# Optimization experiments

Hardware: AMD Instinct MI355X
Metric: run time of the kernel (lower is better)

The kernel has to match this reference:

```python
import jax, jax.numpy as jnp
import numpy as np

B, T, D_IN, H, D_ENC, P, D_ATT = 64, 20, 512, 512, 2048, 196, 512


def setup_inputs() -> dict:
    key = jax.random.key(0)
    ks = jax.random.split(key, 12)
    s = 0.05  # weight scale to keep gates out of saturation
    return {
        "x": jax.random.normal(ks[0], (B, T, D_IN), jnp.float32),
        "cnn_features": jax.random.normal(ks[1], (B, P, D_ENC), jnp.float32),
        "Wi": jax.random.normal(ks[2], (D_IN + H + D_ENC, H), jnp.float32) * s,
        "bi": jnp.zeros((H,), jnp.float32),
        "Wf": jax.random.normal(ks[3], (D_IN + H + D_ENC, H), jnp.float32) * s,
        "bf": jnp.zeros((H,), jnp.float32),
        "Wc": jax.random.normal(ks[4], (D_IN + H + D_ENC, H), jnp.float32) * s,
        "bc": jnp.zeros((H,), jnp.float32),
        "Wo": jax.random.normal(ks[5], (D_IN + H + D_ENC, H), jnp.float32) * s,
        "bo": jnp.zeros((H,), jnp.float32),
        "Wa_feat": jax.random.normal(ks[6], (D_ENC, D_ATT), jnp.float32) * s,
        "Wa_h": jax.random.normal(ks[7], (H, D_ATT), jnp.float32) * s,
        "ba": jnp.zeros((D_ATT,), jnp.float32),
        "v": jax.random.normal(ks[8], (D_ATT,), jnp.float32) * s,
    }


def reference(x, cnn_features, Wi, bi, Wf, bf, Wc, bc, Wo, bo, Wa_feat, Wa_h, ba, v):
    batch, seq_len, _ = x.shape
    hid = Wi.shape[1]
    # feature projection is h-independent: hoist out of the time loop
    feat_proj = jnp.einsum('bpe,ea->bpa', cnn_features, Wa_feat) + ba  # [B,P,A]

    def step(carry, x_t):
        h, c = carry
        # additive (Bahdanau) attention over pixels
        e = jnp.einsum('bpa,a->bp', jnp.tanh(feat_proj + (h @ Wa_h)[:, None, :]), v)
        alpha = jax.nn.softmax(e, axis=-1)                      # [B,P]
        ctx = jnp.einsum('bp,bpe->be', alpha, cnn_features)     # [B,E]
        comb = jnp.concatenate([x_t, h, ctx], axis=1)           # [B,D_IN+H+E]
        i_t = jax.nn.sigmoid(comb @ Wi + bi)
        f_t = jax.nn.sigmoid(comb @ Wf + bf)
        o_t = jax.nn.sigmoid(comb @ Wo + bo)
        c_tilde = jnp.tanh(comb @ Wc + bc)
        c_new = f_t * c + i_t * c_tilde
        h_new = o_t * jnp.tanh(c_new)
        return (h_new, c_new), h_new

    h0 = jnp.zeros((batch, hid), x.dtype)
    c0 = jnp.zeros((batch, hid), x.dtype)
    (h_T, c_T), ys = jax.lax.scan(step, (h0, c0), jnp.swapaxes(x, 0, 1))
    outputs = jnp.swapaxes(ys, 0, 1)  # [B,T,H]
    return outputs, h_T, c_T
```

## Files before the change

kernel.cpp:

```cpp
#include <hip/hip_runtime.h>

typedef unsigned short u16;
typedef unsigned int u32;
typedef __attribute__((ext_vector_type(8))) short bf16x8;
typedef __attribute__((ext_vector_type(4))) float f32x4;

#define NB 64
#define NT 20
#define NH 512
#define NP 196
#define NE 2048
#define NA 512

__device__ __forceinline__ u16 f2bf(float f) {
  u32 b = __float_as_uint(f);
  return (u16)((b + 0x7FFFu + ((b >> 16) & 1u)) >> 16);
}
__device__ __forceinline__ float bf2f(u16 u) { return __uint_as_float(((u32)u) << 16); }
__device__ __forceinline__ float tanh_fast(float x) {
  float xc = fminf(fmaxf(x, -15.f), 15.f);
  float e2 = __builtin_amdgcn_exp2f(xc * 2.885390082f);
  return (e2 - 1.f) * __builtin_amdgcn_rcpf(e2 + 1.f);
}
__device__ __forceinline__ float sigmoid_fast(float x) {
  return __builtin_amdgcn_rcpf(1.f + __builtin_amdgcn_exp2f(x * -1.44269504f));
}

__global__ __launch_bounds__(256) void conv_bf16(const float4* __restrict__ src,
                                                 u16* __restrict__ dst, int n4) {
  int i = blockIdx.x * 256 + threadIdx.x;
  int stride = gridDim.x * 256;
  for (; i < n4; i += stride) {
    float4 v = src[i];
    u32 lo = (u32)f2bf(v.x) | ((u32)f2bf(v.y) << 16);
    u32 hi = (u32)f2bf(v.z) | ((u32)f2bf(v.w) << 16);
    *(uint2*)(dst + (size_t)i * 4) = make_uint2(lo, hi);
  }
}

__global__ __launch_bounds__(128) void conv_x(const float* __restrict__ x,
                                              u16* __restrict__ xbT) {
  int b = blockIdx.x, t = blockIdx.y, tid = threadIdx.x;
  float4 v = *(const float4*)(x + ((size_t)b * NT + t) * 512 + tid * 4);
  u32 lo = (u32)f2bf(v.x) | ((u32)f2bf(v.y) << 16);
  u32 hi = (u32)f2bf(v.z) | ((u32)f2bf(v.w) << 16);
  *(uint2*)(xbT + ((size_t)t * NB + b) * 512 + tid * 4) = make_uint2(lo, hi);
}

__global__ __launch_bounds__(256) void transpose_w(const float* __restrict__ W0,
                                                   const float* __restrict__ W1,
                                                   const float* __restrict__ W2,
                                                   const float* __restrict__ W3,
                                                   u16* __restrict__ dst, int row_off, int K) {
  const float* src = blockIdx.z == 0 ? W0 : blockIdx.z == 1 ? W1 : blockIdx.z == 2 ? W2 : W3;
  __shared__ float tile[32][33];
  int k0 = blockIdx.x * 32, n0 = blockIdx.y * 32;
  int tx = threadIdx.x & 31, ty = threadIdx.x >> 5;
#pragma unroll
  for (int i = 0; i < 4; ++i)
    tile[ty + i * 8][tx] = src[(size_t)(row_off + k0 + ty + i * 8) * 512 + n0 + tx];
  __syncthreads();
#pragma unroll
  for (int i = 0; i < 4; ++i) {
    int n = n0 + ty + i * 8, k = k0 + tx;
    dst[((size_t)blockIdx.z * 512 + n) * K + k] = f2bf(tile[tx][ty + i * 8]);
  }
}

template <bool OUT_BF16, bool BIAS, bool REMAP>
__global__ __launch_bounds__(256) void gemm_bf16(const u16* __restrict__ A,
                                                 const u16* __restrict__ BT,
                                                 const float* __restrict__ bias,
                                                 void* __restrict__ Cout, int M, int N, int K) {
  __shared__ u16 lA[128 * 64];
  __shared__ u16 lB[128 * 64];
  const int tid = threadIdx.x;
  const int lane = tid & 63;
  const int wid = tid >> 6;
  const int m0 = blockIdx.x * 128, n0 = blockIdx.y * 128;
  const int wm = (wid >> 1) * 64, wn = (wid & 1) * 64;
  f32x4 acc[4][4] = {};

  for (int k0 = 0; k0 < K; k0 += 64) {
    __syncthreads();
#pragma unroll
    for (int it = 0; it < 4; ++it) {
      int c = tid + it * 256;
      int r = c >> 3, c7 = c & 7;
      uint4 va = *(const uint4*)(A + (size_t)(m0 + r) * K + k0 + c7 * 8);
      uint4 vb = *(const uint4*)(BT + (size_t)(n0 + r) * K + k0 + c7 * 8);
      int ldsoff = r * 64 + ((c7 ^ (r & 7)) * 8);
      *(uint4*)(lA + ldsoff) = va;
      *(uint4*)(lB + ldsoff) = vb;
    }
    __syncthreads();
#pragma unroll
    for (int kk = 0; kk < 2; ++kk) {
      int kchunk = kk * 4 + (lane >> 4);
      bf16x8 af[4], bg[4];
#pragma unroll
      for (int i = 0; i < 4; ++i) {
        int row = wm + i * 16 + (lane & 15);
        af[i] = *(const bf16x8*)(lA + row * 64 + ((kchunk ^ (row & 7)) * 8));
        int rowb = wn + i * 16 + (lane & 15);
        bg[i] = *(const bf16x8*)(lB + rowb * 64 + ((kchunk ^ (rowb & 7)) * 8));
      }
#pragma unroll
      for (int i = 0; i < 4; ++i)
#pragma unroll
        for (int j = 0; j < 4; ++j)
          acc[i][j] = __builtin_amdgcn_mfma_f32_16x16x32_bf16(af[i], bg[j], acc[i][j], 0, 0, 0);
    }
  }
#pragma unroll
  for (int i = 0; i < 4; ++i) {
    int m = m0 + wm + i * 16 + ((lane >> 4) * 4);
#pragma unroll
    for (int j = 0; j < 4; ++j) {
      int n = n0 + wn + j * 16 + (lane & 15);
      float bv = BIAS ? bias[n] : 0.f;
#pragma unroll
      for (int r = 0; r < 4; ++r) {
        float val = acc[i][j][r] + bv;
        if (REMAP) {
          u32 me = (u32)(m + r);
          u32 bdx = me / 196u;
          u32 p = me - bdx * 196u;
          u32 g = (u32)n >> 9;
          u32 n9 = (u32)n & 511u;
          ((u16*)Cout)[(((size_t)bdx * 4 + g) * 196 + p) * 512 + n9] = f2bf(val);
        } else if (OUT_BF16) {
          ((u16*)Cout)[(size_t)(m + r) * N + n] = f2bf(val);
        } else {
          ((float*)Cout)[(size_t)(m + r) * N + n] = val;
        }
      }
    }
  }
}

__global__ __launch_bounds__(256) void hproj(const u16* __restrict__ hprev,
                                             const u16* __restrict__ wcT,
                                             float* __restrict__ hp) {
  const int ntile = blockIdx.x;
  const int tid = threadIdx.x, lane = tid & 63, kh = tid >> 6;
  const int l15 = lane & 15;
  const u16* Bp = wcT + (size_t)(ntile * 16 + l15) * 512 + kh * 128 + ((lane >> 4) * 8);
  const u16* Ap = hprev + (size_t)l15 * 512 + kh * 128 + ((lane >> 4) * 8);
  f32x4 acc[4] = {};
#pragma unroll
  for (int ks = 0; ks < 4; ++ks) {
    bf16x8 bb = *(const bf16x8*)(Bp + ks * 32);
#pragma unroll
    for (int mf = 0; mf < 4; ++mf) {
      bf16x8 a = *(const bf16x8*)(Ap + (size_t)mf * 16 * 512 + ks * 32);
      acc[mf] = __builtin_amdgcn_mfma_f32_16x16x32_bf16(a, bb, acc[mf], 0, 0, 0);
    }
  }
  __shared__ float pre[4][64][16];
  const int rrow = (lane >> 4) * 4;
#pragma unroll
  for (int mf = 0; mf < 4; ++mf)
#pragma unroll
    for (int r = 0; r < 4; ++r) pre[kh][mf * 16 + rrow + r][l15] = acc[mf][r];
  __syncthreads();
  const int m = tid >> 2, n = (tid & 3) * 4;
  float4 s;
  float* sp = (float*)&s;
#pragma unroll
  for (int j = 0; j < 4; ++j)
    sp[j] = pre[0][m][n + j] + pre[1][m][n + j] + pre[2][m][n + j] + pre[3][m][n + j];
  *(float4*)(hp + (size_t)m * 2560 + ntile * 16 + n) = s;
}

__global__ __launch_bounds__(1024) void attn_gates(
    const u16* __restrict__ fpb, const float* __restrict__ hp, const float* __restrict__ v,
    const u16* __restrict__ cw, const float* __restrict__ xw, const float* __restrict__ bi,
    const float* __restrict__ bfg, const float* __restrict__ bc, const float* __restrict__ bo,
    float* __restrict__ cbuf, float* __restrict__ out, u16* __restrict__ hnext, int t) {
  const int b = blockIdx.x & 63;
  const int half = blockIdx.x >> 6;
  const int tid = threadIdx.x;
  const int lane = tid & 63, wid = tid >> 6;
  __shared__ float smem_a[1024];
  __shared__ float sm[256];
  __shared__ float alp[200];
  __shared__ float red[8192];

  float* hwa = smem_a;
  float* vv = smem_a + 512;
  if (tid < 512) {
    hwa[tid] = (t > 0) ? hp[(size_t)b * 2560 + 2048 + tid] : 0.f;
    vv[tid] = v[tid];
  }
  if (tid >= 196 && tid < 256) red[tid] = -3e38f;
  __syncthreads();

  float hw[8], vr[8];
#pragma unroll
  for (int j = 0; j < 8; ++j) {
    hw[j] = hwa[lane * 8 + j];
    vr[j] = vv[lane * 8 + j];
  }
  for (int p = wid; p < NP; p += 16) {
    const u16* fp = fpb + ((size_t)b * NP + p) * 512 + lane * 8;
    uint4 raw = *(const uint4*)fp;
    u32 w[4] = {raw.x, raw.y, raw.z, raw.w};
    float part = 0.f;
#pragma unroll
    for (int j = 0; j < 8; ++j) {
      u16 u = (u16)(w[j >> 1] >> ((j & 1) * 16));
      part += tanh_fast(bf2f(u) + hw[j]) * vr[j];
    }
#pragma unroll
    for (int off = 32; off > 0; off >>= 1) part += __shfl_xor(part, off);
    if (lane == 0) red[p] = part;
  }
  __syncthreads();

  float ev = (tid < 256) ? red[tid] : -3e38f;
  if (tid < 256) sm[tid] = ev;
  __syncthreads();
  for (int s = 128; s > 0; s >>= 1) {
    if (tid < s) sm[tid] = fmaxf(sm[tid], sm[tid + s]);
    __syncthreads();
  }
  float mx = sm[0];
  __syncthreads();
  float w = (tid < NP) ? __builtin_amdgcn_exp2f((ev - mx) * 1.44269504f) : 0.f;
  if (tid < 256) sm[tid] = w;
  __syncthreads();
  for (int s = 128; s > 0; s >>= 1) {
    if (tid < s) sm[tid] += sm[tid + s];
    __syncthreads();
  }
  float inv = __builtin_amdgcn_rcpf(sm[0]);
  if (tid < NP) alp[tid] = w * inv;
  __syncthreads();

  {
    const int g = tid >> 8, pg = (tid >> 5) & 7, colc = tid & 31;
    const u16* base = cw + ((size_t)(b * 4 + g) * 196) * 512 + half * 256 + colc * 8;
    float acc[8] = {};
    for (int i = 0; i < 25; ++i) {
      int p = pg + i * 8;
      if (p < NP) {
        float al = alp[p];
        uint4 raw = *(const uint4*)(base + (size_t)p * 512);
        u32 wds[4] = {raw.x, raw.y, raw.z, raw.w};
#pragma unroll
        for (int j = 0; j < 8; ++j) acc[j] += al * bf2f((u16)(wds[j >> 1] >> ((j & 1) * 16)));
      }
    }
#pragma unroll
    for (int j = 0; j < 8; ++j) red[((g * 8 + pg) * 32 + colc) * 8 + j] = acc[j];
  }
  __syncthreads();

  float* pre4 = smem_a;
  {
    const int g = tid >> 8, nn = tid & 255;
    float s = 0.f;
#pragma unroll
    for (int pg = 0; pg < 8; ++pg) s += red[((g * 8 + pg) * 32 + (nn >> 3)) * 8 + (nn & 7)];
    pre4[g * 256 + nn] = s;
  }
  __syncthreads();

  if (tid < 256) {
    const int ng = half * 256 + tid;
    const size_t xwo = ((size_t)t * NB + b) * 2048;
    const size_t hpb = (size_t)b * 2560;
    float hwh0 = 0.f, hwh1 = 0.f, hwh2 = 0.f, hwh3 = 0.f;
    if (t > 0) {
      hwh0 = hp[hpb + ng];
      hwh1 = hp[hpb + 512 + ng];
      hwh2 = hp[hpb + 1024 + ng];
      hwh3 = hp[hpb + 1536 + ng];
    }
    float ip = pre4[0 * 256 + tid] + xw[xwo + ng] + hwh0 + bi[ng];
    float fp = pre4[1 * 256 + tid] + xw[xwo + 512 + ng] + hwh1 + bfg[ng];
    float cp = pre4[2 * 256 + tid] + xw[xwo + 1024 + ng] + hwh2 + bc[ng];
    float op = pre4[3 * 256 + tid] + xw[xwo + 1536 + ng] + hwh3 + bo[ng];
    float it = sigmoid_fast(ip), ft = sigmoid_fast(fp), ot = sigmoid_fast(op);
    float ctl = tanh_fast(cp);
    float cold = (t > 0) ? cbuf[(size_t)b * 512 + ng] : 0.f;
    float cn = ft * cold + it * ctl;
    float hn = ot * tanh_fast(cn);
    cbuf[(size_t)b * 512 + ng] = cn;
    hnext[(size_t)b * 512 + ng] = f2bf(hn);
    out[((size_t)b * NT + t) * 512 + ng] = hn;
    if (t == NT - 1) {
      out[(size_t)NB * NT * 512 + (size_t)b * 512 + ng] = hn;
      out[(size_t)NB * NT * 512 + (size_t)NB * 512 + (size_t)b * 512 + ng] = cn;
    }
  }
}

extern "C" void kernel_launch(void* const* d_in, const int* in_sizes, int n_in, void* d_out,
                              int out_size, void* d_ws, size_t ws_size, hipStream_t stream) {
  const float* x = (const float*)d_in[0];
  const float* cnn = (const float*)d_in[1];
  const float* Wi = (const float*)d_in[2];
  const float* bi = (const float*)d_in[3];
  const float* Wf = (const float*)d_in[4];
  const float* bfv = (const float*)d_in[5];
  const float* Wc = (const float*)d_in[6];
  const float* bc = (const float*)d_in[7];
  const float* Wo = (const float*)d_in[8];
  const float* bo = (const float*)d_in[9];
  const float* Waf = (const float*)d_in[10];
  const float* Wah = (const float*)d_in[11];
  const float* ba = (const float*)d_in[12];
  const float* v = (const float*)d_in[13];
  float* out = (float*)d_out;

  char* base = (char*)d_ws;
  size_t off = 0;
  auto alloc = [&](size_t bytes) {
    char* r = base + off;
    off += (bytes + 255) & ~(size_t)255;
    return r;
  };
  u16* cnnb = (u16*)alloc((size_t)NB * NP * NE * 2);
  u16* fpb = (u16*)alloc((size_t)NB * NP * NA * 2);
  u16* cnW = (u16*)alloc((size_t)NB * 4 * NP * 512 * 2);
  u16* wctxT = (u16*)alloc((size_t)4 * 512 * 2048 * 2);
  u16* wcombT = (u16*)alloc((size_t)2560 * 512 * 2);
  u16* wxt = (u16*)alloc((size_t)4 * 512 * 512 * 2);
  u16* waft = (u16*)alloc((size_t)512 * 2048 * 2);
  u16* xbT = (u16*)alloc((size_t)NT * NB * 512 * 2);
  float* xw = (float*)alloc((size_t)NT * NB * 2048 * 4);
  u16* hbuf = (u16*)alloc((size_t)2 * NB * 512 * 2);
  float* cbuf = (float*)alloc((size_t)NB * 512 * 4);
  float* hp = (float*)alloc((size_t)NB * 2560 * 4);

  (void)ws_size;
  (void)in_sizes;
  (void)n_in;
  (void)out_size;

  conv_bf16<<<2048, 256, 0, stream>>>((const float4*)cnn, cnnb, (NB * NP * NE) / 4);
  conv_x<<<dim3(NB, NT), 128, 0, stream>>>(x, xbT);
  {
    dim3 g1(512 / 32, 16, 4);
    transpose_w<<<g1, 256, 0, stream>>>(Wi, Wf, Wc, Wo, wxt, 0, 512);
    dim3 g2(2048 / 32, 16, 1);
    transpose_w<<<g2, 256, 0, stream>>>(Waf, Waf, Waf, Waf, waft, 0, 2048);
    dim3 g3(2048 / 32, 16, 4);
    transpose_w<<<g3, 256, 0, stream>>>(Wi, Wf, Wc, Wo, wctxT, 1024, 2048);
    dim3 g4(512 / 32, 16, 4);
    transpose_w<<<g4, 256, 0, stream>>>(Wi, Wf, Wc, Wo, wcombT, 512, 512);
    dim3 g5(512 / 32, 16, 1);
    transpose_w<<<g5, 256, 0, stream>>>(Wah, Wah, Wah, Wah, wcombT + (size_t)2048 * 512, 0, 512);
  }

  {
    dim3 g(12544 / 128, 512 / 128);
    gemm_bf16<true, true, false><<<g, 256, 0, stream>>>(cnnb, waft, ba, fpb, 12544, 512, 2048);
  }
  {
    dim3 g(1280 / 128, 2048 / 128);
    gemm_bf16<false, false, false><<<g, 256, 0, stream>>>(xbT, wxt, nullptr, xw, 1280, 2048, 512);
  }
  {
    dim3 g(12544 / 128, 2048 / 128);
    gemm_bf16<true, false, true><<<g, 256, 0, stream>>>(cnnb, wctxT, nullptr, cnW, 12544, 2048,
                                                        2048);
  }

  for (int t = 0; t < NT; ++t) {
    const u16* hprev = hbuf + (size_t)(t & 1) * NB * 512;
    u16* hnext = hbuf + (size_t)((t + 1) & 1) * NB * 512;
    if (t > 0) hproj<<<160, 256, 0, stream>>>(hprev, wcombT, hp);
    attn_gates<<<128, 1024, 0, stream>>>(fpb, hp, v, cnW, xw, bi, bfv, bc, bo, cbuf, out, hnext,
                                         t);
  }
}
```

Baseline: 763.7 us.

## Merge feature and context GEMMs, use direct global-to-LDS loads, shuffle softmax

Concatenates the transposed Wa_feat and context-gate weights into one 2560-wide matrix so the two large GEMMs over the bf16 CNN features become a single launch with a split epilogue. The GEMM tile loads now use global_load_lds to write straight into LDS, skipping the round trip through registers, with swizzled source addresses precomputed outside the k loop. The attention softmax replaces its shared-memory tree reductions with wavefront shuffle reductions, cutting the number of barriers. The merged GEMM reads the A operand once instead of twice but adds a branch to its epilogue, and the direct-to-LDS path depends on the swizzled layout still matching what the MFMA fragment reads expect.

```diff
diff --git a/kernel.cpp b/kernel.cpp
--- a/kernel.cpp
+++ b/kernel.cpp
@@ -24,6 +24,11 @@
 }
 __device__ __forceinline__ float sigmoid_fast(float x) {
   return __builtin_amdgcn_rcpf(1.f + __builtin_amdgcn_exp2f(x * -1.44269504f));
+}
+
+__device__ __forceinline__ void gload_lds16(const u16* g, u16* l) {
+  __builtin_amdgcn_global_load_lds((const __attribute__((address_space(1))) void*)g,
+                                   (__attribute__((address_space(3))) void*)l, 16, 0, 0);
 }
 
 __global__ __launch_bounds__(256) void conv_bf16(const float4* __restrict__ src,
@@ -67,11 +72,12 @@
   }
 }
 
-template <bool OUT_BF16, bool BIAS, bool REMAP>
+template <bool MERGED, bool OUT_BF16, bool BIAS>
 __global__ __launch_bounds__(256) void gemm_bf16(const u16* __restrict__ A,
                                                  const u16* __restrict__ BT,
                                                  const float* __restrict__ bias,
-                                                 void* __restrict__ Cout, int M, int N, int K) {
+                                                 void* __restrict__ C0, u16* __restrict__ C1,
+                                                 int M, int N, int K) {
   __shared__ u16 lA[128 * 64];
   __shared__ u16 lB[128 * 64];
   const int tid = threadIdx.x;
@@ -81,17 +87,23 @@
   const int wm = (wid >> 1) * 64, wn = (wid & 1) * 64;
   f32x4 acc[4][4] = {};
 
+  const int cbase = wid * 256;
+  int srcr[4], srcc[4];
+#pragma unroll
+  for (int it = 0; it < 4; ++it) {
+    int c = cbase + it * 64 + lane;
+    srcr[it] = c >> 3;
+    srcc[it] = ((c & 7) ^ ((c >> 3) & 7)) * 8;
+  }
+
   for (int k0 = 0; k0 < K; k0 += 64) {
     __syncthreads();
 #pragma unroll
     for (int it = 0; it < 4; ++it) {
-      int c = tid + it * 256;
-      int r = c >> 3, c7 = c & 7;
-      uint4 va = *(const uint4*)(A + (size_t)(m0 + r) * K + k0 + c7 * 8);
-      uint4 vb = *(const uint4*)(BT + (size_t)(n0 + r) * K + k0 + c7 * 8);
-      int ldsoff = r * 64 + ((c7 ^ (r & 7)) * 8);
-      *(uint4*)(lA + ldsoff) = va;
-      *(uint4*)(lB + ldsoff) = vb;
+      const u16* sA = A + (size_t)(m0 + srcr[it]) * K + k0 + srcc[it];
+      const u16* sB = BT + (size_t)(n0 + srcr[it]) * K + k0 + srcc[it];
+      gload_lds16(sA, lA + (size_t)(cbase + it * 64) * 8);
+      gload_lds16(sB, lB + (size_t)(cbase + it * 64) * 8);
     }
     __syncthreads();
 #pragma unroll
@@ -118,21 +130,26 @@
 #pragma unroll
     for (int j = 0; j < 4; ++j) {
       int n = n0 + wn + j * 16 + (lane & 15);
-      float bv = BIAS ? bias[n] : 0.f;
+      float bv = 0.f;
+      if (BIAS && (!MERGED || n < 512)) bv = bias[n];
 #pragma unroll
       for (int r = 0; r < 4; ++r) {
         float val = acc[i][j][r] + bv;
-        if (REMAP) {
+        if (MERGED) {
           u32 me = (u32)(m + r);
-          u32 bdx = me / 196u;
-          u32 p = me - bdx * 196u;
-          u32 g = (u32)n >> 9;
-          u32 n9 = (u32)n & 511u;
-          ((u16*)Cout)[(((size_t)bdx * 4 + g) * 196 + p) * 512 + n9] = f2bf(val);
+          if (n < 512) {
+            ((u16*)C0)[(size_t)me * 512 + n] = f2bf(val);
+          } else {
+            u32 bdx = me / 196u;
+            u32 p = me - bdx * 196u;
+            u32 g = (u32)(n - 512) >> 9;
+            u32 n9 = (u32)(n - 512) & 511u;
+            C1[(((size_t)bdx * 4 + g) * 196 + p) * 512 + n9] = f2bf(val);
+          }
         } else if (OUT_BF16) {
-          ((u16*)Cout)[(size_t)(m + r) * N + n] = f2bf(val);
+          ((u16*)C0)[(size_t)(m + r) * N + n] = f2bf(val);
         } else {
-          ((float*)Cout)[(size_t)(m + r) * N + n] = val;
+          ((float*)C0)[(size_t)(m + r) * N + n] = val;
         }
       }
     }
@@ -183,7 +200,7 @@
   const int tid = threadIdx.x;
   const int lane = tid & 63, wid = tid >> 6;
   __shared__ float smem_a[1024];
-  __shared__ float sm[256];
+  __shared__ float sm[16];
   __shared__ float alp[200];
   __shared__ float red[8192];
 
@@ -218,24 +235,28 @@
   }
   __syncthreads();
 
-  float ev = (tid < 256) ? red[tid] : -3e38f;
-  if (tid < 256) sm[tid] = ev;
-  __syncthreads();
-  for (int s = 128; s > 0; s >>= 1) {
-    if (tid < s) sm[tid] = fmaxf(sm[tid], sm[tid + s]);
-    __syncthreads();
-  }
-  float mx = sm[0];
-  __syncthreads();
-  float w = (tid < NP) ? __builtin_amdgcn_exp2f((ev - mx) * 1.44269504f) : 0.f;
-  if (tid < 256) sm[tid] = w;
-  __syncthreads();
-  for (int s = 128; s > 0; s >>= 1) {
-    if (tid < s) sm[tid] += sm[tid + s];
-    __syncthreads();
-  }
-  float inv = __builtin_amdgcn_rcpf(sm[0]);
-  if (tid < NP) alp[tid] = w * inv;
+  float ev = 0.f, w = 0.f;
+  if (tid < 256) {
+    ev = red[tid];
+    float m_ = ev;
+#pragma unroll
+    for (int off = 32; off > 0; off >>= 1) m_ = fmaxf(m_, __shfl_xor(m_, off));
+    if (lane == 0) sm[wid] = m_;
+  }
+  __syncthreads();
+  if (tid < 256) {
+    float mx = fmaxf(fmaxf(sm[0], sm[1]), fmaxf(sm[2], sm[3]));
+    w = (tid < NP) ? __builtin_amdgcn_exp2f((ev - mx) * 1.44269504f) : 0.f;
+    float s_ = w;
+#pragma unroll
+    for (int off = 32; off > 0; off >>= 1) s_ += __shfl_xor(s_, off);
+    if (lane == 0) sm[8 + wid] = s_;
+  }
+  __syncthreads();
+  if (tid < NP) {
+    float tot = (sm[8] + sm[9]) + (sm[10] + sm[11]);
+    alp[tid] = w * __builtin_amdgcn_rcpf(tot);
+  }
   __syncthreads();
 
   {
@@ -325,10 +346,9 @@
   u16* cnnb = (u16*)alloc((size_t)NB * NP * NE * 2);
   u16* fpb = (u16*)alloc((size_t)NB * NP * NA * 2);
   u16* cnW = (u16*)alloc((size_t)NB * 4 * NP * 512 * 2);
-  u16* wctxT = (u16*)alloc((size_t)4 * 512 * 2048 * 2);
+  u16* wbig = (u16*)alloc((size_t)2560 * 2048 * 2);
   u16* wcombT = (u16*)alloc((size_t)2560 * 512 * 2);
   u16* wxt = (u16*)alloc((size_t)4 * 512 * 512 * 2);
-  u16* waft = (u16*)alloc((size_t)512 * 2048 * 2);
   u16* xbT = (u16*)alloc((size_t)NT * NB * 512 * 2);
   float* xw = (float*)alloc((size_t)NT * NB * 2048 * 4);
   u16* hbuf = (u16*)alloc((size_t)2 * NB * 512 * 2);
@@ -346,9 +366,9 @@
     dim3 g1(512 / 32, 16, 4);
     transpose_w<<<g1, 256, 0, stream>>>(Wi, Wf, Wc, Wo, wxt, 0, 512);
     dim3 g2(2048 / 32, 16, 1);
-    transpose_w<<<g2, 256, 0, stream>>>(Waf, Waf, Waf, Waf, waft, 0, 2048);
+    transpose_w<<<g2, 256, 0, stream>>>(Waf, Waf, Waf, Waf, wbig, 0, 2048);
     dim3 g3(2048 / 32, 16, 4);
-    transpose_w<<<g3, 256, 0, stream>>>(Wi, Wf, Wc, Wo, wctxT, 1024, 2048);
+    transpose_w<<<g3, 256, 0, stream>>>(Wi, Wf, Wc, Wo, wbig + (size_t)512 * 2048, 1024, 2048);
     dim3 g4(512 / 32, 16, 4);
     transpose_w<<<g4, 256, 0, stream>>>(Wi, Wf, Wc, Wo, wcombT, 512, 512);
     dim3 g5(512 / 32, 16, 1);
@@ -356,17 +376,14 @@
   }
 
   {
-    dim3 g(12544 / 128, 512 / 128);
-    gemm_bf16<true, true, false><<<g, 256, 0, stream>>>(cnnb, waft, ba, fpb, 12544, 512, 2048);
+    dim3 g(12544 / 128, 2560 / 128);
+    gemm_bf16<true, true, true><<<g, 256, 0, stream>>>(cnnb, wbig, ba, fpb, cnW, 12544, 2560,
+                                                       2048);
   }
   {
     dim3 g(1280 / 128, 2048 / 128);
-    gemm_bf16<false, false, false><<<g, 256, 0, stream>>>(xbT, wxt, nullptr, xw, 1280, 2048, 512);
-  }
-  {
-    dim3 g(12544 / 128, 2048 / 128);
-    gemm_bf16<true, false, true><<<g, 256, 0, stream>>>(cnnb, wctxT, nullptr, cnW, 12544, 2048,
-                                                        2048);
+    gemm_bf16<false, false, false><<<g, 256, 0, stream>>>(xbT, wxt, nullptr, xw, nullptr, 1280,
+                                                          2048, 512);
   }
 
   for (int t = 0; t < NT; ++t) {
```

After: 739.1 us. 1.03x faster.
